# Kernel optimization log

Measured on AMD Instinct MI355X. Metric: run time of the kernel, lower is better.

## Reference

```python
import jax, jax.numpy as jnp
import numpy as np
from jax import lax

B, C_IN, T = 64, 16, 8192
HID, OUT = 64, 10
NEW_T = T // 4            # two MaxPool1d(2)
N_NODES = B * NEW_T       # 131072
N_EDGES = 2_097_152       # avg degree 16


def setup_inputs() -> dict:
    key = jax.random.key(0)
    ks = jax.random.split(key, 8)
    x = jax.random.normal(ks[0], (B, C_IN, T), dtype=jnp.float32)
    edge_index = jax.random.randint(ks[1], (2, N_EDGES), 0, N_NODES, dtype=jnp.int32)
    s = 0.05
    return {
        "x": x,
        "edge_index": edge_index,
        "conv1_w": jax.random.normal(ks[2], (16, C_IN, 5), dtype=jnp.float32) * s,
        "conv1_b": jnp.zeros((16,), jnp.float32),
        "conv2_w": jax.random.normal(ks[3], (32, 16, 5), dtype=jnp.float32) * s,
        "conv2_b": jnp.zeros((32,), jnp.float32),
        "gcn1_w": jax.random.normal(ks[4], (32, HID), dtype=jnp.float32) * s,
        "gcn1_b": jnp.zeros((HID,), jnp.float32),
        "gcn2_w": jax.random.normal(ks[5], (HID, HID), dtype=jnp.float32) * s,
        "gcn2_b": jnp.zeros((HID,), jnp.float32),
        "cls_w": jax.random.normal(ks[6], (HID, OUT), dtype=jnp.float32) * s,
        "cls_b": jnp.zeros((OUT,), jnp.float32),
    }


def conv1d(x, w, b):
    # x: [B, Cin, T], w: [Cout, Cin, K], padding=2 -> same length
    y = lax.conv_general_dilated(x, w, window_strides=(1,), padding=[(2, 2)],
                                 dimension_numbers=("NCH", "OIH", "NCH"))
    return y + b[None, :, None]


def maxpool2(x):
    # non-overlapping MaxPool1d(kernel=2) over last dim
    b, c, t = x.shape
    return x.reshape(b, c, t // 2, 2).max(axis=-1)


def gcn_conv(x, edge_index, W, b, n):
    # PyG GCNConv: add self-loops, symmetric normalization, scatter-add aggregate
    row, col = edge_index[0], edge_index[1]   # source j, target i
    loop = jnp.arange(n, dtype=row.dtype)
    row = jnp.concatenate([row, loop])
    col = jnp.concatenate([col, loop])
    deg = jax.ops.segment_sum(jnp.ones(row.shape, x.dtype), col, num_segments=n)
    dis = jnp.where(deg > 0, lax.rsqrt(deg), jnp.zeros_like(deg))
    norm = dis[row] * dis[col]                # [E+N]
    xw = x @ W                                # [N, out]
    msg = xw[row] * norm[:, None]             # gather along edges
    out = jax.ops.segment_sum(msg, col, num_segments=n)
    return out + b


def reference(x, edge_index, conv1_w, conv1_b, conv2_w, conv2_b,
              gcn1_w, gcn1_b, gcn2_w, gcn2_b, cls_w, cls_b):
    h = maxpool2(jax.nn.relu(conv1d(x, conv1_w, conv1_b)))     # [B,16,T/2]
    h = maxpool2(jax.nn.relu(conv1d(h, conv2_w, conv2_b)))     # [B,32,T/4]
    feat = h.transpose(0, 2, 1).reshape(-1, 32)                # [B*new_T, 32]
    n = feat.shape[0]
    g = jax.nn.relu(gcn_conv(feat, edge_index, gcn1_w, gcn1_b, n))
    g = jax.nn.relu(gcn_conv(g, edge_index, gcn2_w, gcn2_b, n))
    pooled = g.reshape(B, -1, HID).mean(axis=1)                # [B, HID]
    return pooled @ cls_w + cls_b                               # [B, OUT]
```

## Files before the change

### kernel.cpp

```cpp
#include <hip/hip_runtime.h>
#include <hip/hip_bf16.h>
#include <hip/hip_fp16.h>

#define BATCH 64
#define C_IN 16
#define T0 8192
#define T1 4096
#define T2 2048
#define N_NODES (BATCH * T2)
#define HID 64
#define NOUT 10

#define NCB 256
#define CB_SHIFT 9
#define CB_TGT 512
#define RCAP 9216
#define PC_EDGES 2048
#define PC_CAP 28

#define PK_RMASK 0x1FFFF

#define EC 1024

#define ZROW N_NODES

#define ROWW 24

#define FP8_SCALE 256.0f
#define FP8_SINV  (1.0f / 256.0f)

typedef __fp16 half8 __attribute__((ext_vector_type(8)));
typedef __fp16 half4v __attribute__((ext_vector_type(4)));
typedef float floatx4 __attribute__((ext_vector_type(4)));
typedef float floatx2 __attribute__((ext_vector_type(2)));

__global__ __launch_bounds__(256) void conv1_partition(
    const float* __restrict__ x, const float* __restrict__ w,
    const float* __restrict__ bias, __fp16* __restrict__ h1,
    const int* __restrict__ ei, int E,
    int* __restrict__ rcnt, int* __restrict__ gpairs,
    float* __restrict__ pool, unsigned char* __restrict__ xw,
    unsigned char* __restrict__ xw2) {
  __shared__ int smem_i[NCB + NCB * PC_CAP];
  if ((blockIdx.x & 1) == 0) {
    __fp16* xs = (__fp16*)smem_i;
    int bid = blockIdx.x >> 1;
    int b = bid >> 4;
    int tp0 = (bid & 15) * 256;
    if (bid == 0) {
      for (int k = threadIdx.x; k < BATCH * HID; k += 256) pool[k] = 0.f;
      if (threadIdx.x < 16) {
        ((unsigned*)(xw + (size_t)ZROW * 64))[threadIdx.x] = 0u;
        ((unsigned*)(xw2 + (size_t)ZROW * 64))[threadIdx.x] = 0u;
      }
    }
    int t_base = 2 * tp0 - 8;
    const float* xb = x + (size_t)b * C_IN * T0;
    {
      int ci = threadIdx.x >> 4;
      int l16 = threadIdx.x & 15;
      const float* xrow = xb + ci * T0;
      float4 va[4];
#pragma unroll
      for (int k = 0; k < 4; ++k) {
        int c4 = l16 + k * 16;
        int gt = t_base + c4 * 4;
        va[k] = make_float4(0.f, 0.f, 0.f, 0.f);
        if (gt >= 0 && gt + 4 <= T0) va[k] = *(const float4*)(xrow + gt);
      }
#pragma unroll
      for (int k = 0; k < 4; ++k) {
        int c4 = l16 + k * 16;
        __fp16* d = xs + (c4 * 4) * ROWW + ci;
        d[0] = (__fp16)va[k].x;
        d[ROWW] = (__fp16)va[k].y;
        d[2 * ROWW] = (__fp16)va[k].z;
        d[3 * ROWW] = (__fp16)va[k].w;
      }
      float4 vb[5];
      int okb[5];
#pragma unroll
      for (int k = 0; k < 5; ++k) {
        int c4 = l16 + (4 + k) * 16;
        okb[k] = (c4 < 132);
        int gt = t_base + c4 * 4;
        vb[k] = make_float4(0.f, 0.f, 0.f, 0.f);
        if (okb[k] && gt >= 0 && gt + 4 <= T0) vb[k] = *(const float4*)(xrow + gt);
      }
#pragma unroll
      for (int k = 0; k < 5; ++k) {
        if (okb[k]) {
          int c4 = l16 + (4 + k) * 16;
          __fp16* d = xs + (c4 * 4) * ROWW + ci;
          d[0] = (__fp16)vb[k].x;
          d[ROWW] = (__fp16)vb[k].y;
          d[2 * ROWW] = (__fp16)vb[k].z;
          d[3 * ROWW] = (__fp16)vb[k].w;
        }
      }
    }
    int ln = threadIdx.x & 15;
    int q = (threadIdx.x & 63) >> 4;
    int wib = threadIdx.x >> 6;
    half8 wb[3];
#pragma unroll
    for (int ks = 0; ks < 3; ++ks) {
      int kk = ks * 2 + (q >> 1);
#pragma unroll
      for (int j = 0; j < 8; ++j) {
        int ci = (q & 1) * 8 + j;
        float wv = (kk < 5) ? w[(ln * 16 + ci) * 5 + kk] : 0.f;
        wb[ks][j] = (__fp16)wv;
      }
    }
    float bv = bias[ln];
    __syncthreads();
    int qh = q >> 1, qo = (q & 1) * 8;
#pragma unroll 2
    for (int mtl = 0; mtl < 8; ++mtl) {
      int mt = wib * 8 + mtl;
      int posb = mt * 16 + ln + qh + 6;
      half8 a0 = *(const half8*)(xs + posb * ROWW + qo);
      half8 a1 = *(const half8*)(xs + (posb + 2) * ROWW + qo);
      half8 a2 = *(const half8*)(xs + (posb + 4) * ROWW + qo);
      floatx4 c0 = {0.f, 0.f, 0.f, 0.f};
      c0 = __builtin_amdgcn_mfma_f32_16x16x32_f16(a0, wb[0], c0, 0, 0, 0);
      c0 = __builtin_amdgcn_mfma_f32_16x16x32_f16(a1, wb[1], c0, 0, 0, 0);
      c0 = __builtin_amdgcn_mfma_f32_16x16x32_f16(a2, wb[2], c0, 0, 0, 0);
      int tp = tp0 + mt * 8 + q * 2;
      size_t o = ((size_t)b * T1 + tp) * 16 + ln;
      h1[o] = (__fp16)fmaxf(fmaxf(c0[0], c0[1]) + bv, 0.f);
      h1[o + 16] = (__fp16)fmaxf(fmaxf(c0[2], c0[3]) + bv, 0.f);
    }
  } else {
    int* lcnt = smem_i;
    int* lpk = smem_i + NCB;
    int pid = blockIdx.x >> 1;
    if (threadIdx.x < NCB) lcnt[threadIdx.x] = 0;
    __syncthreads();
    int e0 = pid * PC_EDGES;
    int rr[8], cc[8];
#pragma unroll
    for (int j = 0; j < 8; ++j) {
      int e = e0 + j * 256 + threadIdx.x;
      rr[j] = (e < E) ? ei[e] : 0;
      cc[j] = (e < E) ? ei[E + e] : -1;
    }
#pragma unroll
    for (int j = 0; j < 8; ++j) {
      if (cc[j] >= 0) {
        int cb = cc[j] >> CB_SHIFT;
        int pk = rr[j] | ((cc[j] & (CB_TGT - 1)) << 17);
        int slot = atomicAdd(&lcnt[cb], 1);
        if (slot < PC_CAP) {
          lpk[cb * PC_CAP + slot] = pk;
        } else {
          int pos = atomicAdd(&rcnt[cb], 1);
          if (pos < RCAP) gpairs[(size_t)cb * RCAP + pos] = pk;
        }
      }
    }
    __syncthreads();
    int t = threadIdx.x;
    if (t < NCB) {
      int n = lcnt[t];
      if (n > PC_CAP) n = PC_CAP;
      if (n > 0) {
        int base = atomicAdd(&rcnt[t], n);
        int* dst = gpairs + (size_t)t * RCAP;
        for (int k = 0; k < n; ++k) {
          int p = base + k;
          if (p < RCAP) dst[p] = lpk[t * PC_CAP + k];
        }
      }
    }
  }
}

__global__ __launch_bounds__(256) void conv2_gemm1(const __fp16* __restrict__ h1,
    const float* __restrict__ w, const float* __restrict__ bias,
    const float* __restrict__ W1, const float* __restrict__ dis,
    unsigned char* __restrict__ xw) {
  __shared__ __fp16 xs[520 * ROWW];
  __shared__ __fp16 fs[256 * 40];
  int b = blockIdx.x >> 3;
  int tp0 = (blockIdx.x & 7) * 256;
  int t_base = 2 * tp0 - 2;
  {
    half8 v[5];
    int row_[5], hf_[5], ok_[5];
#pragma unroll
    for (int k = 0; k < 5; ++k) {
      int idx = threadIdx.x + k * 256;
      ok_[k] = (idx < 520 * 2);
      int row = idx >> 1, hf = idx & 1;
      int gt = t_base + row;
      half8 z;
#pragma unroll
      for (int j = 0; j < 8; ++j) z[j] = (__fp16)0.f;
      v[k] = z;
      if (ok_[k] && gt >= 0 && gt < T1)
        v[k] = *(const half8*)(h1 + ((size_t)b * T1 + gt) * 16 + hf * 8);
      row_[k] = row; hf_[k] = hf;
    }
#pragma unroll
    for (int k = 0; k < 5; ++k)
      if (ok_[k]) *(half8*)(xs + row_[k] * ROWW + hf_[k] * 8) = v[k];
  }
  int ln = threadIdx.x & 15;
  int q = (threadIdx.x & 63) >> 4;
  int wib = threadIdx.x >> 6;
  half8 wb[2][3];
#pragma unroll
  for (int nt = 0; nt < 2; ++nt)
#pragma unroll
    for (int ks = 0; ks < 3; ++ks) {
      int kk = ks * 2 + (q >> 1);
#pragma unroll
      for (int j = 0; j < 8; ++j) {
        int ci = (q & 1) * 8 + j;
        float wv = (kk < 5) ? w[((nt * 16 + ln) * 16 + ci) * 5 + kk] : 0.f;
        wb[nt][ks][j] = (__fp16)wv;
      }
    }
  float b20 = bias[ln];
  float b21 = bias[16 + ln];
  __syncthreads();
  int qh = q >> 1, qo = (q & 1) * 8;
#pragma unroll 2
  for (int mtl = 0; mtl < 8; ++mtl) {
    int mt = wib * 8 + mtl;
    int posb = mt * 16 + ln + qh;
    half8 a0 = *(const half8*)(xs + posb * ROWW + qo);
    half8 a1 = *(const half8*)(xs + (posb + 2) * ROWW + qo);
    half8 a2 = *(const half8*)(xs + (posb + 4) * ROWW + qo);
    floatx4 c0 = {0.f, 0.f, 0.f, 0.f};
    floatx4 c1 = {0.f, 0.f, 0.f, 0.f};
    c0 = __builtin_amdgcn_mfma_f32_16x16x32_f16(a0, wb[0][0], c0, 0, 0, 0);
    c0 = __builtin_amdgcn_mfma_f32_16x16x32_f16(a1, wb[0][1], c0, 0, 0, 0);
    c0 = __builtin_amdgcn_mfma_f32_16x16x32_f16(a2, wb[0][2], c0, 0, 0, 0);
    c1 = __builtin_amdgcn_mfma_f32_16x16x32_f16(a0, wb[1][0], c1, 0, 0, 0);
    c1 = __builtin_amdgcn_mfma_f32_16x16x32_f16(a1, wb[1][1], c1, 0, 0, 0);
    c1 = __builtin_amdgcn_mfma_f32_16x16x32_f16(a2, wb[1][2], c1, 0, 0, 0);
    int node = wib * 64 + mtl * 8 + q * 2;
    fs[node * 40 + ln] = (__fp16)fmaxf(fmaxf(c0[0], c0[1]) + b20, 0.f);
    fs[(node + 1) * 40 + ln] = (__fp16)fmaxf(fmaxf(c0[2], c0[3]) + b20, 0.f);
    fs[node * 40 + 16 + ln] = (__fp16)fmaxf(fmaxf(c1[0], c1[1]) + b21, 0.f);
    fs[(node + 1) * 40 + 16 + ln] = (__fp16)fmaxf(fmaxf(c1[2], c1[3]) + b21, 0.f);
  }
  half8 bf[4];
#pragma unroll
  for (int t = 0; t < 4; ++t)
#pragma unroll
    for (int j = 0; j < 8; ++j)
      bf[t][j] = (__fp16)W1[(q * 8 + j) * 64 + ln * 4 + t];
  int gnode0 = b * T2 + tp0;
#pragma unroll
  for (int tt = 0; tt < 4; ++tt) {
    int lbase = (wib * 4 + tt) * 16;
    half8 a = *(const half8*)(fs + (lbase + ln) * 40 + q * 8);
    float d[4];
#pragma unroll
    for (int r = 0; r < 4; ++r) d[r] = dis[gnode0 + lbase + q * 4 + r] * FP8_SCALE;
    floatx4 acc[4];
#pragma unroll
    for (int t = 0; t < 4; ++t) {
      floatx4 z = {0.f, 0.f, 0.f, 0.f};
      acc[t] = __builtin_amdgcn_mfma_f32_16x16x32_f16(a, bf[t], z, 0, 0, 0);
    }
#pragma unroll
    for (int r = 0; r < 4; ++r) {
      int u = __builtin_amdgcn_cvt_pk_fp8_f32(acc[0][r] * d[r], acc[1][r] * d[r], 0, 0);
      u = __builtin_amdgcn_cvt_pk_fp8_f32(acc[2][r] * d[r], acc[3][r] * d[r], u, 1);
      *(unsigned*)(xw + (size_t)(gnode0 + lbase + q * 4 + r) * 64 + ln * 4) = (unsigned)u;
    }
  }
}

__global__ __launch_bounds__(512) void build_csr(const int* __restrict__ gpairs,
    const int* __restrict__ rcnt, int* __restrict__ ebuf,
    int* __restrict__ estart, int* __restrict__ ecnt, float* __restrict__ dis) {
  __shared__ int deg[CB_TGT];
  __shared__ int cur[CB_TGT];
  __shared__ int sc[CB_TGT];
  __shared__ int wsum[8];
  int b = blockIdx.x;
  int t = threadIdx.x;
  deg[t] = 0;
  cur[t] = 0;
  __syncthreads();
  int m = rcnt[b];
  if (m > RCAP) m = RCAP;
  const int* reg = gpairs + (size_t)b * RCAP;
  for (int k0 = 0; k0 < m; k0 += 2048) {
    int p[4], have[4];
#pragma unroll
    for (int u = 0; u < 4; ++u) {
      int k = k0 + u * 512 + t;
      have[u] = (k < m);
      p[u] = have[u] ? reg[k] : 0;
    }
#pragma unroll
    for (int u = 0; u < 4; ++u)
      if (have[u]) atomicAdd(&deg[(p[u] >> 17) & (CB_TGT - 1)], 1);
  }
  __syncthreads();
  int d = deg[t];
  int lane = t & 63;
  int wv = t >> 6;
  int sum = d;
#pragma unroll
  for (int off = 1; off < 64; off <<= 1) {
    int v = __shfl_up(sum, off, 64);
    if (lane >= off) sum += v;
  }
  if (lane == 63) wsum[wv] = sum;
  __syncthreads();
  int prefix = 0;
#pragma unroll
  for (int i = 0; i < 8; ++i) prefix += (i < wv) ? wsum[i] : 0;
  int excl = prefix + sum - d;
  int gi = (b << CB_SHIFT) + t;
  int base = b * RCAP;
  estart[gi] = base + excl;
  ecnt[gi] = d;
  dis[gi] = rsqrtf((float)d + 1.0f);
  sc[t] = excl;
  __syncthreads();
  for (int k0 = 0; k0 < m; k0 += 2048) {
    int p[4], have[4];
#pragma unroll
    for (int u = 0; u < 4; ++u) {
      int k = k0 + u * 512 + t;
      have[u] = (k < m);
      p[u] = have[u] ? reg[k] : 0;
    }
#pragma unroll
    for (int u = 0; u < 4; ++u) {
      if (have[u]) {
        int lc = (p[u] >> 17) & (CB_TGT - 1);
        int off = atomicAdd(&cur[lc], 1);
        ebuf[base + sc[lc] + off] = p[u] & PK_RMASK;
      }
    }
  }
}

#define LOADW(dst_, b0_)                                                        \
  _Pragma("unroll")                                                             \
  for (int j = 0; j < 4; ++j) {                                                 \
    unsigned r = (unsigned)sidx[(b0_) + j * 4];                                 \
    dst_[j] = *(const unsigned*)(tab + ((r << 6) + ch4));                       \
  }
#define LOADWT(dst_, stl_, s0_, c_)                                             \
  _Pragma("unroll")                                                             \
  for (int j = 0; j < 4; ++j) {                                                 \
    int k = (s0_) + j * 4 + es;                                                 \
    unsigned r = (unsigned)sidx[(stl_) + k];                                    \
    unsigned off = (k < (c_)) ? ((r << 6) + ch4) : zoff;                        \
    dst_[j] = *(const unsigned*)(tab + off);                                    \
  }
#define CONSW(src_, ALO, AHI)                                                   \
  _Pragma("unroll")                                                             \
  for (int j = 0; j < 4; ++j) {                                                 \
    ALO += __builtin_amdgcn_cvt_pk_f32_fp8(src_[j], 0);                         \
    AHI += __builtin_amdgcn_cvt_pk_f32_fp8(src_[j], 1);                         \
  }
#define GATHER_NODE(c_, stl_, ALO, AHI)                                         \
  {                                                                             \
    int sb_ = (stl_) + es;                                                      \
    int nt_ = ((c_) + 15) >> 4;                                                 \
    int nf_ = (c_) >> 4;                                                        \
    unsigned wa_[4], wb_[4];                                                    \
    if (nt_ > 0) {                                                              \
      if (nf_ > 0) { LOADW(wa_, sb_) } else { LOADWT(wa_, stl_, 0, c_) }        \
    }                                                                           \
    for (int w_ = 0; w_ < nt_; ++w_) {                                          \
      int n_ = w_ + 1;                                                          \
      if (n_ < nt_) {                                                           \
        if (w_ & 1) {                                                           \
          if (n_ < nf_) { LOADW(wa_, sb_ + (n_ << 4)) }                         \
          else { LOADWT(wa_, stl_, n_ << 4, c_) }                               \
        } else {                                                                \
          if (n_ < nf_) { LOADW(wb_, sb_ + (n_ << 4)) }                         \
          else { LOADWT(wb_, stl_, n_ << 4, c_) }                               \
        }                                                                       \
      }                                                                         \
      if (w_ & 1) { CONSW(wb_, ALO, AHI) } else { CONSW(wa_, ALO, AHI) }        \
    }                                                                           \
  }

#define STAGE_SIDX()                                                            \
  {                                                                             \
    int v0 = 0, v1 = 0, v2 = 0, v3 = 0;                                         \
    if (t < total) v0 = ebuf[span0 + t];                                        \
    if (t + 256 < total) v1 = ebuf[span0 + t + 256];                            \
    if (t + 512 < total) v2 = ebuf[span0 + t + 512];                            \
    if (t + 768 < total) v3 = ebuf[span0 + t + 768];                            \
    if (t < total) sidx[t] = v0;                                                \
    if (t + 256 < total) sidx[t + 256] = v1;                                    \
    if (t + 512 < total) sidx[t + 512] = v2;                                    \
    if (t + 768 < total) sidx[t + 768] = v3;                                    \
  }

__global__ __launch_bounds__(256) void agg1_gemm2(const unsigned char* __restrict__ tab,
    const int* __restrict__ ebuf, const int* __restrict__ estart,
    const int* __restrict__ ecnt, const float* __restrict__ dis,
    const float* __restrict__ bias, const float* __restrict__ W2,
    unsigned char* __restrict__ xw2, int N) {
  __shared__ __fp16 g1s[16 * 72];
  __shared__ int sidx[EC + 16];
  __shared__ int sst[16], scn[16];
  int t = threadIdx.x;
  int base16 = blockIdx.x * 16;
  if (t < 16) {
    sst[t] = estart[base16 + t];
    scn[t] = ecnt[base16 + t];
  }
  __syncthreads();
  int span0 = sst[0];
  int total = sst[15] + scn[15] - span0;
  if (total > EC) total = EC;
  STAGE_SIDX()
  __syncthreads();
  int lane = t & 63;
  int es = lane >> 4;
  int ch = lane & 15;
  int wib = t >> 6;
  unsigned ch4 = (unsigned)ch * 4u;
  unsigned zoff = ((unsigned)ZROW << 6) + ch4;
  float4 bv = *(const float4*)(bias + ch * 4);
  half8 b0, b1;
#pragma unroll
  for (int j = 0; j < 8; ++j) {
    b0[j] = (__fp16)W2[((lane >> 4) * 8 + j) * 64 + wib * 16 + (lane & 15)];
    b1[j] = (__fp16)W2[(32 + (lane >> 4) * 8 + j) * 64 + wib * 16 + (lane & 15)];
  }
  unsigned swv[4];
#pragma unroll
  for (int jj = 0; jj < 4; ++jj)
    swv[jj] = *(const unsigned*)(tab + (((unsigned)(base16 + wib * 4 + jj) << 6) + ch4));
#pragma unroll
  for (int jj = 0; jj < 4; ++jj) {
    int il = wib * 4 + jj;
    int i = base16 + il;
    int stl = sst[il] - span0;
    int c = scn[il];
    if (stl + c > EC) c = (EC > stl) ? (EC - stl) : 0;
    float di = dis[i] * FP8_SINV;
    floatx2 aLO = {0.f, 0.f}, aHI = {0.f, 0.f};
    GATHER_NODE(c, stl, aLO, aHI)
    float ax = aLO.x, ay = aLO.y, az = aHI.x, aw = aHI.y;
    ax += __shfl_xor(ax, 16, 64); ax += __shfl_xor(ax, 32, 64);
    ay += __shfl_xor(ay, 16, 64); ay += __shfl_xor(ay, 32, 64);
    az += __shfl_xor(az, 16, 64); az += __shfl_xor(az, 32, 64);
    aw += __shfl_xor(aw, 16, 64); aw += __shfl_xor(aw, 32, 64);
    floatx2 slo = __builtin_amdgcn_cvt_pk_f32_fp8(swv[jj], 0);
    floatx2 shi = __builtin_amdgcn_cvt_pk_f32_fp8(swv[jj], 1);
    if (es == 0) {
      half4v r;
      r[0] = (__fp16)fmaxf((ax + slo.x) * di + bv.x, 0.f);
      r[1] = (__fp16)fmaxf((ay + slo.y) * di + bv.y, 0.f);
      r[2] = (__fp16)fmaxf((az + shi.x) * di + bv.z, 0.f);
      r[3] = (__fp16)fmaxf((aw + shi.y) * di + bv.w, 0.f);
      *(half4v*)(g1s + il * 72 + ch * 4) = r;
    }
  }
  __syncthreads();
  int m = lane & 15;
  int q = lane >> 4;
  half8 a0 = *(const half8*)(g1s + m * 72 + q * 8);
  half8 a1 = *(const half8*)(g1s + m * 72 + 32 + q * 8);
  floatx4 acc = {0.f, 0.f, 0.f, 0.f};
  acc = __builtin_amdgcn_mfma_f32_16x16x32_f16(a0, b0, acc, 0, 0, 0);
  acc = __builtin_amdgcn_mfma_f32_16x16x32_f16(a1, b1, acc, 0, 0, 0);
  float sv[4];
#pragma unroll
  for (int r = 0; r < 4; ++r)
    sv[r] = acc[r] * dis[base16 + q * 4 + r] * FP8_SCALE;
  int u = __builtin_amdgcn_cvt_pk_fp8_f32(sv[0], sv[1], 0, 0);
  u = __builtin_amdgcn_cvt_pk_fp8_f32(sv[2], sv[3], u, 1);
#pragma unroll
  for (int r = 0; r < 4; ++r) {
    int node = base16 + q * 4 + r;
    xw2[(size_t)node * 64 + wib * 16 + m] = (unsigned char)(((unsigned)u) >> (8 * r));
  }
}

__global__ __launch_bounds__(256) void gcn_aggregate_pool(const unsigned char* __restrict__ tab,
    const int* __restrict__ ebuf, const int* __restrict__ estart,
    const int* __restrict__ ecnt, const float* __restrict__ dis,
    const float* __restrict__ bias, float* __restrict__ pool, int N) {
  __shared__ float4 red[4][16];
  __shared__ int sidx[EC + 16];
  __shared__ int sst[16], scn[16];
  int t = threadIdx.x;
  int base16 = blockIdx.x * 16;
  if (t < 16) {
    sst[t] = estart[base16 + t];
    scn[t] = ecnt[base16 + t];
  }
  __syncthreads();
  int span0 = sst[0];
  int total = sst[15] + scn[15] - span0;
  if (total > EC) total = EC;
  STAGE_SIDX()
  __syncthreads();
  int lane = t & 63;
  int es = lane >> 4;
  int ch = lane & 15;
  int wib = t >> 6;
  unsigned ch4 = (unsigned)ch * 4u;
  unsigned zoff = ((unsigned)ZROW << 6) + ch4;
  float4 bv = *(const float4*)(bias + ch * 4);
  unsigned swv[4];
#pragma unroll
  for (int jj = 0; jj < 4; ++jj)
    swv[jj] = *(const unsigned*)(tab + (((unsigned)(base16 + wib * 4 + jj) << 6) + ch4));
  float px = 0.f, py = 0.f, pz = 0.f, pw = 0.f;
#pragma unroll
  for (int jj = 0; jj < 4; ++jj) {
    int il = wib * 4 + jj;
    int i = base16 + il;
    int stl = sst[il] - span0;
    int c = scn[il];
    if (stl + c > EC) c = (EC > stl) ? (EC - stl) : 0;
    float di = dis[i] * FP8_SINV;
    floatx2 aLO = {0.f, 0.f}, aHI = {0.f, 0.f};
    GATHER_NODE(c, stl, aLO, aHI)
    float ax = aLO.x, ay = aLO.y, az = aHI.x, aw = aHI.y;
    ax += __shfl_xor(ax, 16, 64); ax += __shfl_xor(ax, 32, 64);
    ay += __shfl_xor(ay, 16, 64); ay += __shfl_xor(ay, 32, 64);
    az += __shfl_xor(az, 16, 64); az += __shfl_xor(az, 32, 64);
    aw += __shfl_xor(aw, 16, 64); aw += __shfl_xor(aw, 32, 64);
    floatx2 slo = __builtin_amdgcn_cvt_pk_f32_fp8(swv[jj], 0);
    floatx2 shi = __builtin_amdgcn_cvt_pk_f32_fp8(swv[jj], 1);
    px += fmaxf((ax + slo.x) * di + bv.x, 0.f);
    py += fmaxf((ay + slo.y) * di + bv.y, 0.f);
    pz += fmaxf((az + shi.x) * di + bv.z, 0.f);
    pw += fmaxf((aw + shi.y) * di + bv.w, 0.f);
  }
  if (es == 0) red[wib][ch] = make_float4(px, py, pz, pw);
  __syncthreads();
  if (threadIdx.x < 64) {
    int f = threadIdx.x;
    int c4 = f >> 2, j4 = f & 3;
    const float* r0 = (const float*)&red[0][c4];
    const float* r1 = (const float*)&red[1][c4];
    const float* r2 = (const float*)&red[2][c4];
    const float* r3 = (const float*)&red[3][c4];
    float sum = r0[j4] + r1[j4] + r2[j4] + r3[j4];
    int b = (blockIdx.x * 16) >> 11;
    atomicAdd(&pool[b * 64 + f], sum);
  }
}

__global__ __launch_bounds__(64) void classify(const float* __restrict__ pool,
    const float* __restrict__ cw, const float* __restrict__ cb,
    float* __restrict__ out) {
  __shared__ float pl[64];
  int b = blockIdx.x;
  int t = threadIdx.x;
  pl[t] = pool[b * 64 + t] * (1.0f / (float)T2);
  __syncthreads();
  if (t < NOUT) {
    float a = cb[t];
#pragma unroll
    for (int k = 0; k < 64; ++k) a += pl[k] * cw[k * NOUT + t];
    out[b * NOUT + t] = a;
  }
}

extern "C" void kernel_launch(void* const* d_in, const int* in_sizes, int n_in,
                              void* d_out, int out_size, void* d_ws, size_t ws_size,
                              hipStream_t stream) {
  const float* x    = (const float*)d_in[0];
  const int*   ei   = (const int*)d_in[1];
  const float* c1w  = (const float*)d_in[2];
  const float* c1b  = (const float*)d_in[3];
  const float* c2w  = (const float*)d_in[4];
  const float* c2b  = (const float*)d_in[5];
  const float* g1w  = (const float*)d_in[6];
  const float* g1b  = (const float*)d_in[7];
  const float* g2w  = (const float*)d_in[8];
  const float* g2b  = (const float*)d_in[9];
  const float* cw   = (const float*)d_in[10];
  const float* cb   = (const float*)d_in[11];
  float* out = (float*)d_out;
  int E = in_sizes[1] / 2;
  const int N = N_NODES;

  char* ws = (char*)d_ws;
  int*    gpairs = (int*)(ws);
  int*    ebuf   = (int*)(ws + 9437184);
  int*    rcnt   = (int*)(ws + 18874368);
  int*    estart = (int*)(ws + 18878464);
  int*    ecnt   = (int*)(ws + 19402752);
  float*  dis    = (float*)(ws + 19927040);
  float*  pool   = (float*)(ws + 20451328);
  unsigned char* xw  = (unsigned char*)(ws + 20467712);
  unsigned char* xw2 = (unsigned char*)(ws + 37245184);
  __fp16* h1     = (__fp16*)(ws + 54022656);

  hipMemsetAsync(rcnt, 0, NCB * sizeof(int), stream);

  conv1_partition<<<dim3(BATCH * 16 * 2), dim3(256), 0, stream>>>(
      x, c1w, c1b, h1, ei, E, rcnt, gpairs, pool, xw, xw2);

  build_csr<<<dim3(NCB), dim3(512), 0, stream>>>(gpairs, rcnt, ebuf, estart, ecnt, dis);

  conv2_gemm1<<<dim3(BATCH * 8), dim3(256), 0, stream>>>(h1, c2w, c2b, g1w, dis, xw);
  agg1_gemm2<<<dim3(N / 16), dim3(256), 0, stream>>>(xw, ebuf, estart, ecnt, dis, g1b, g2w, xw2, N);
  gcn_aggregate_pool<<<dim3(N / 16), dim3(256), 0, stream>>>(xw2, ebuf, estart, ecnt, dis, g2b, pool, N);

  classify<<<dim3(BATCH), dim3(64), 0, stream>>>(pool, cw, cb, out);
}
```

Before: 246.1 us.

## Fuse CSR build with conv2+GEMM1 via global degree atomics

```diff
diff --git a/kernel.cpp b/kernel.cpp
--- a/kernel.cpp
+++ b/kernel.cpp
@@ -39,6 +39,7 @@
     const float* __restrict__ bias, __fp16* __restrict__ h1,
     const int* __restrict__ ei, int E,
     int* __restrict__ rcnt, int* __restrict__ gpairs,
+    int* __restrict__ deg_g,
     float* __restrict__ pool, unsigned char* __restrict__ xw,
     unsigned char* __restrict__ xw2) {
   __shared__ int smem_i[NCB + NCB * PC_CAP];
@@ -127,7 +128,8 @@
       c0 = __builtin_amdgcn_mfma_f32_16x16x32_f16(a0, wb[0], c0, 0, 0, 0);
       c0 = __builtin_amdgcn_mfma_f32_16x16x32_f16(a1, wb[1], c0, 0, 0, 0);
       c0 = __builtin_amdgcn_mfma_f32_16x16x32_f16(a2, wb[2], c0, 0, 0, 0);
-      int tp = tp0 + mt * 8 + q * 2;
+      int tp = tp0 + mtl * 8 + q * 2 + wib * 64;
+      tp = tp0 + mt * 8 + q * 2;
       size_t o = ((size_t)b * T1 + tp) * 16 + ln;
       h1[o] = (__fp16)fmaxf(fmaxf(c0[0], c0[1]) + bv, 0.f);
       h1[o + 16] = (__fp16)fmaxf(fmaxf(c0[2], c0[3]) + bv, 0.f);
@@ -149,6 +151,7 @@
 #pragma unroll
     for (int j = 0; j < 8; ++j) {
       if (cc[j] >= 0) {
+        atomicAdd(&deg_g[cc[j]], 1);
         int cb = cc[j] >> CB_SHIFT;
         int pk = rr[j] | ((cc[j] & (CB_TGT - 1)) << 17);
         int slot = atomicAdd(&lcnt[cb], 1);
@@ -177,170 +180,176 @@
   }
 }
 
-__global__ __launch_bounds__(256) void conv2_gemm1(const __fp16* __restrict__ h1,
-    const float* __restrict__ w, const float* __restrict__ bias,
-    const float* __restrict__ W1, const float* __restrict__ dis,
-    unsigned char* __restrict__ xw) {
-  __shared__ __fp16 xs[520 * ROWW];
-  __shared__ __fp16 fs[256 * 40];
-  int b = blockIdx.x >> 3;
-  int tp0 = (blockIdx.x & 7) * 256;
-  int t_base = 2 * tp0 - 2;
-  {
-    half8 v[5];
-    int row_[5], hf_[5], ok_[5];
-#pragma unroll
-    for (int k = 0; k < 5; ++k) {
-      int idx = threadIdx.x + k * 256;
-      ok_[k] = (idx < 520 * 2);
-      int row = idx >> 1, hf = idx & 1;
-      int gt = t_base + row;
-      half8 z;
-#pragma unroll
-      for (int j = 0; j < 8; ++j) z[j] = (__fp16)0.f;
-      v[k] = z;
-      if (ok_[k] && gt >= 0 && gt < T1)
-        v[k] = *(const half8*)(h1 + ((size_t)b * T1 + gt) * 16 + hf * 8);
-      row_[k] = row; hf_[k] = hf;
-    }
-#pragma unroll
-    for (int k = 0; k < 5; ++k)
-      if (ok_[k]) *(half8*)(xs + row_[k] * ROWW + hf_[k] * 8) = v[k];
-  }
-  int ln = threadIdx.x & 15;
-  int q = (threadIdx.x & 63) >> 4;
-  int wib = threadIdx.x >> 6;
-  half8 wb[2][3];
-#pragma unroll
-  for (int nt = 0; nt < 2; ++nt)
-#pragma unroll
-    for (int ks = 0; ks < 3; ++ks) {
-      int kk = ks * 2 + (q >> 1);
-#pragma unroll
-      for (int j = 0; j < 8; ++j) {
-        int ci = (q & 1) * 8 + j;
-        float wv = (kk < 5) ? w[((nt * 16 + ln) * 16 + ci) * 5 + kk] : 0.f;
-        wb[nt][ks][j] = (__fp16)wv;
-      }
-    }
-  float b20 = bias[ln];
-  float b21 = bias[16 + ln];
-  __syncthreads();
-  int qh = q >> 1, qo = (q & 1) * 8;
-#pragma unroll 2
-  for (int mtl = 0; mtl < 8; ++mtl) {
-    int mt = wib * 8 + mtl;
-    int posb = mt * 16 + ln + qh;
-    half8 a0 = *(const half8*)(xs + posb * ROWW + qo);
-    half8 a1 = *(const half8*)(xs + (posb + 2) * ROWW + qo);
-    half8 a2 = *(const half8*)(xs + (posb + 4) * ROWW + qo);
-    floatx4 c0 = {0.f, 0.f, 0.f, 0.f};
-    floatx4 c1 = {0.f, 0.f, 0.f, 0.f};
-    c0 = __builtin_amdgcn_mfma_f32_16x16x32_f16(a0, wb[0][0], c0, 0, 0, 0);
-    c0 = __builtin_amdgcn_mfma_f32_16x16x32_f16(a1, wb[0][1], c0, 0, 0, 0);
-    c0 = __builtin_amdgcn_mfma_f32_16x16x32_f16(a2, wb[0][2], c0, 0, 0, 0);
-    c1 = __builtin_amdgcn_mfma_f32_16x16x32_f16(a0, wb[1][0], c1, 0, 0, 0);
-    c1 = __builtin_amdgcn_mfma_f32_16x16x32_f16(a1, wb[1][1], c1, 0, 0, 0);
-    c1 = __builtin_amdgcn_mfma_f32_16x16x32_f16(a2, wb[1][2], c1, 0, 0, 0);
-    int node = wib * 64 + mtl * 8 + q * 2;
-    fs[node * 40 + ln] = (__fp16)fmaxf(fmaxf(c0[0], c0[1]) + b20, 0.f);
-    fs[(node + 1) * 40 + ln] = (__fp16)fmaxf(fmaxf(c0[2], c0[3]) + b20, 0.f);
-    fs[node * 40 + 16 + ln] = (__fp16)fmaxf(fmaxf(c1[0], c1[1]) + b21, 0.f);
-    fs[(node + 1) * 40 + 16 + ln] = (__fp16)fmaxf(fmaxf(c1[2], c1[3]) + b21, 0.f);
-  }
-  half8 bf[4];
-#pragma unroll
-  for (int t = 0; t < 4; ++t)
-#pragma unroll
-    for (int j = 0; j < 8; ++j)
-      bf[t][j] = (__fp16)W1[(q * 8 + j) * 64 + ln * 4 + t];
-  int gnode0 = b * T2 + tp0;
-#pragma unroll
-  for (int tt = 0; tt < 4; ++tt) {
-    int lbase = (wib * 4 + tt) * 16;
-    half8 a = *(const half8*)(fs + (lbase + ln) * 40 + q * 8);
-    float d[4];
-#pragma unroll
-    for (int r = 0; r < 4; ++r) d[r] = dis[gnode0 + lbase + q * 4 + r] * FP8_SCALE;
-    floatx4 acc[4];
-#pragma unroll
-    for (int t = 0; t < 4; ++t) {
-      floatx4 z = {0.f, 0.f, 0.f, 0.f};
-      acc[t] = __builtin_amdgcn_mfma_f32_16x16x32_f16(a, bf[t], z, 0, 0, 0);
-    }
-#pragma unroll
-    for (int r = 0; r < 4; ++r) {
-      int u = __builtin_amdgcn_cvt_pk_fp8_f32(acc[0][r] * d[r], acc[1][r] * d[r], 0, 0);
-      u = __builtin_amdgcn_cvt_pk_fp8_f32(acc[2][r] * d[r], acc[3][r] * d[r], u, 1);
-      *(unsigned*)(xw + (size_t)(gnode0 + lbase + q * 4 + r) * 64 + ln * 4) = (unsigned)u;
-    }
-  }
-}
-
-__global__ __launch_bounds__(512) void build_csr(const int* __restrict__ gpairs,
+__global__ __launch_bounds__(512) void csr_conv2(const int* __restrict__ gpairs,
     const int* __restrict__ rcnt, int* __restrict__ ebuf,
-    int* __restrict__ estart, int* __restrict__ ecnt, float* __restrict__ dis) {
-  __shared__ int deg[CB_TGT];
-  __shared__ int cur[CB_TGT];
-  __shared__ int sc[CB_TGT];
-  __shared__ int wsum[8];
-  int b = blockIdx.x;
-  int t = threadIdx.x;
-  deg[t] = 0;
-  cur[t] = 0;
-  __syncthreads();
-  int m = rcnt[b];
-  if (m > RCAP) m = RCAP;
-  const int* reg = gpairs + (size_t)b * RCAP;
-  for (int k0 = 0; k0 < m; k0 += 2048) {
-    int p[4], have[4];
-#pragma unroll
-    for (int u = 0; u < 4; ++u) {
-      int k = k0 + u * 512 + t;
-      have[u] = (k < m);
-      p[u] = have[u] ? reg[k] : 0;
-    }
-#pragma unroll
-    for (int u = 0; u < 4; ++u)
-      if (have[u]) atomicAdd(&deg[(p[u] >> 17) & (CB_TGT - 1)], 1);
-  }
-  __syncthreads();
-  int d = deg[t];
-  int lane = t & 63;
-  int wv = t >> 6;
-  int sum = d;
-#pragma unroll
-  for (int off = 1; off < 64; off <<= 1) {
-    int v = __shfl_up(sum, off, 64);
-    if (lane >= off) sum += v;
-  }
-  if (lane == 63) wsum[wv] = sum;
-  __syncthreads();
-  int prefix = 0;
-#pragma unroll
-  for (int i = 0; i < 8; ++i) prefix += (i < wv) ? wsum[i] : 0;
-  int excl = prefix + sum - d;
-  int gi = (b << CB_SHIFT) + t;
-  int base = b * RCAP;
-  estart[gi] = base + excl;
-  ecnt[gi] = d;
-  dis[gi] = rsqrtf((float)d + 1.0f);
-  sc[t] = excl;
-  __syncthreads();
-  for (int k0 = 0; k0 < m; k0 += 2048) {
-    int p[4], have[4];
-#pragma unroll
-    for (int u = 0; u < 4; ++u) {
-      int k = k0 + u * 512 + t;
-      have[u] = (k < m);
-      p[u] = have[u] ? reg[k] : 0;
-    }
-#pragma unroll
-    for (int u = 0; u < 4; ++u) {
-      if (have[u]) {
-        int lc = (p[u] >> 17) & (CB_TGT - 1);
-        int off = atomicAdd(&cur[lc], 1);
-        ebuf[base + sc[lc] + off] = p[u] & PK_RMASK;
+    int* __restrict__ estart, int* __restrict__ ecnt, float* __restrict__ dis,
+    const __fp16* __restrict__ h1, const float* __restrict__ w,
+    const float* __restrict__ bias, const float* __restrict__ W1,
+    const int* __restrict__ deg_g, unsigned char* __restrict__ xw) {
+  __shared__ int smem_i[11616];
+  int bid = blockIdx.x;
+  if (bid % 3 == 0) {
+    int* deg = smem_i;
+    int* cur = smem_i + 512;
+    int* sc = smem_i + 1024;
+    int* wsum = smem_i + 1536;
+    int b = bid / 3;
+    int t = threadIdx.x;
+    deg[t] = 0;
+    cur[t] = 0;
+    __syncthreads();
+    int m = rcnt[b];
+    if (m > RCAP) m = RCAP;
+    const int* reg = gpairs + (size_t)b * RCAP;
+    for (int k0 = 0; k0 < m; k0 += 2048) {
+      int p[4], have[4];
+#pragma unroll
+      for (int u = 0; u < 4; ++u) {
+        int k = k0 + u * 512 + t;
+        have[u] = (k < m);
+        p[u] = have[u] ? reg[k] : 0;
+      }
+#pragma unroll
+      for (int u = 0; u < 4; ++u)
+        if (have[u]) atomicAdd(&deg[(p[u] >> 17) & (CB_TGT - 1)], 1);
+    }
+    __syncthreads();
+    int d = deg[t];
+    int lane = t & 63;
+    int wv = t >> 6;
+    int sum = d;
+#pragma unroll
+    for (int off = 1; off < 64; off <<= 1) {
+      int v = __shfl_up(sum, off, 64);
+      if (lane >= off) sum += v;
+    }
+    if (lane == 63) wsum[wv] = sum;
+    __syncthreads();
+    int prefix = 0;
+#pragma unroll
+    for (int i = 0; i < 8; ++i) prefix += (i < wv) ? wsum[i] : 0;
+    int excl = prefix + sum - d;
+    int gi = (b << CB_SHIFT) + t;
+    int base = b * RCAP;
+    estart[gi] = base + excl;
+    ecnt[gi] = d;
+    dis[gi] = rsqrtf((float)d + 1.0f);
+    sc[t] = excl;
+    __syncthreads();
+    for (int k0 = 0; k0 < m; k0 += 2048) {
+      int p[4], have[4];
+#pragma unroll
+      for (int u = 0; u < 4; ++u) {
+        int k = k0 + u * 512 + t;
+        have[u] = (k < m);
+        p[u] = have[u] ? reg[k] : 0;
+      }
+#pragma unroll
+      for (int u = 0; u < 4; ++u) {
+        if (have[u]) {
+          int lc = (p[u] >> 17) & (CB_TGT - 1);
+          int off = atomicAdd(&cur[lc], 1);
+          ebuf[base + sc[lc] + off] = p[u] & PK_RMASK;
+        }
+      }
+    }
+  } else {
+    __fp16* xs = (__fp16*)smem_i;
+    __fp16* fs = (__fp16*)(smem_i + 6240);
+    float* disl = (float*)(smem_i + 11360);
+    int cid = bid - bid / 3 - 1;
+    int b = cid >> 3;
+    int tp0 = (cid & 7) * 256;
+    int t = threadIdx.x;
+    int t_base = 2 * tp0 - 2;
+    int gnode0 = b * T2 + tp0;
+    if (t < 256) disl[t] = rsqrtf((float)deg_g[gnode0 + t] + 1.0f) * FP8_SCALE;
+    {
+      half8 v[3];
+      int row_[3], hf_[3], ok_[3];
+#pragma unroll
+      for (int k = 0; k < 3; ++k) {
+        int idx = t + k * 512;
+        ok_[k] = (idx < 520 * 2);
+        int row = idx >> 1, hf = idx & 1;
+        int gt = t_base + row;
+        half8 z;
+#pragma unroll
+        for (int j = 0; j < 8; ++j) z[j] = (__fp16)0.f;
+        v[k] = z;
+        if (ok_[k] && gt >= 0 && gt < T1)
+          v[k] = *(const half8*)(h1 + ((size_t)b * T1 + gt) * 16 + hf * 8);
+        row_[k] = row; hf_[k] = hf;
+      }
+#pragma unroll
+      for (int k = 0; k < 3; ++k)
+        if (ok_[k]) *(half8*)(xs + row_[k] * ROWW + hf_[k] * 8) = v[k];
+    }
+    int ln = t & 15;
+    int q = (t & 63) >> 4;
+    int wib = t >> 6;
+    half8 wb[2][3];
+#pragma unroll
+    for (int nt = 0; nt < 2; ++nt)
+#pragma unroll
+      for (int ks = 0; ks < 3; ++ks) {
+        int kk = ks * 2 + (q >> 1);
+#pragma unroll
+        for (int j = 0; j < 8; ++j) {
+          int ci = (q & 1) * 8 + j;
+          float wv = (kk < 5) ? w[((nt * 16 + ln) * 16 + ci) * 5 + kk] : 0.f;
+          wb[nt][ks][j] = (__fp16)wv;
+        }
+      }
+    float b20 = bias[ln];
+    float b21 = bias[16 + ln];
+    __syncthreads();
+    int qh = q >> 1, qo = (q & 1) * 8;
+#pragma unroll
+    for (int mtl = 0; mtl < 4; ++mtl) {
+      int mt = wib * 4 + mtl;
+      int posb = mt * 16 + ln + qh;
+      half8 a0 = *(const half8*)(xs + posb * ROWW + qo);
+      half8 a1 = *(const half8*)(xs + (posb + 2) * ROWW + qo);
+      half8 a2 = *(const half8*)(xs + (posb + 4) * ROWW + qo);
+      floatx4 c0 = {0.f, 0.f, 0.f, 0.f};
+      floatx4 c1 = {0.f, 0.f, 0.f, 0.f};
+      c0 = __builtin_amdgcn_mfma_f32_16x16x32_f16(a0, wb[0][0], c0, 0, 0, 0);
+      c0 = __builtin_amdgcn_mfma_f32_16x16x32_f16(a1, wb[0][1], c0, 0, 0, 0);
+      c0 = __builtin_amdgcn_mfma_f32_16x16x32_f16(a2, wb[0][2], c0, 0, 0, 0);
+      c1 = __builtin_amdgcn_mfma_f32_16x16x32_f16(a0, wb[1][0], c1, 0, 0, 0);
+      c1 = __builtin_amdgcn_mfma_f32_16x16x32_f16(a1, wb[1][1], c1, 0, 0, 0);
+      c1 = __builtin_amdgcn_mfma_f32_16x16x32_f16(a2, wb[1][2], c1, 0, 0, 0);
+      int node = mt * 8 + q * 2;
+      fs[node * 40 + ln] = (__fp16)fmaxf(fmaxf(c0[0], c0[1]) + b20, 0.f);
+      fs[(node + 1) * 40 + ln] = (__fp16)fmaxf(fmaxf(c0[2], c0[3]) + b20, 0.f);
+      fs[node * 40 + 16 + ln] = (__fp16)fmaxf(fmaxf(c1[0], c1[1]) + b21, 0.f);
+      fs[(node + 1) * 40 + 16 + ln] = (__fp16)fmaxf(fmaxf(c1[2], c1[3]) + b21, 0.f);
+    }
+    half8 bf[4];
+#pragma unroll
+    for (int tc = 0; tc < 4; ++tc)
+#pragma unroll
+      for (int j = 0; j < 8; ++j)
+        bf[tc][j] = (__fp16)W1[(q * 8 + j) * 64 + ln * 4 + tc];
+#pragma unroll
+    for (int tt = 0; tt < 2; ++tt) {
+      int lbase = (wib * 2 + tt) * 16;
+      half8 a = *(const half8*)(fs + (lbase + ln) * 40 + q * 8);
+      float d[4];
+#pragma unroll
+      for (int r = 0; r < 4; ++r) d[r] = disl[lbase + q * 4 + r];
+      floatx4 acc[4];
+#pragma unroll
+      for (int tc = 0; tc < 4; ++tc) {
+        floatx4 z = {0.f, 0.f, 0.f, 0.f};
+        acc[tc] = __builtin_amdgcn_mfma_f32_16x16x32_f16(a, bf[tc], z, 0, 0, 0);
+      }
+#pragma unroll
+      for (int r = 0; r < 4; ++r) {
+        int u = __builtin_amdgcn_cvt_pk_fp8_f32(acc[0][r] * d[r], acc[1][r] * d[r], 0, 0);
+        u = __builtin_amdgcn_cvt_pk_fp8_f32(acc[2][r] * d[r], acc[3][r] * d[r], u, 1);
+        *(unsigned*)(xw + (size_t)(gnode0 + lbase + q * 4 + r) * 64 + ln * 4) = (unsigned)u;
       }
     }
   }
@@ -599,17 +608,19 @@
   float*  dis    = (float*)(ws + 19927040);
   float*  pool   = (float*)(ws + 20451328);
   unsigned char* xw  = (unsigned char*)(ws + 20467712);
+  int*    deg_g  = (int*)(ws + 28856384);
   unsigned char* xw2 = (unsigned char*)(ws + 37245184);
   __fp16* h1     = (__fp16*)(ws + 54022656);
 
   hipMemsetAsync(rcnt, 0, NCB * sizeof(int), stream);
+  hipMemsetAsync(deg_g, 0, N_NODES * sizeof(int), stream);
 
   conv1_partition<<<dim3(BATCH * 16 * 2), dim3(256), 0, stream>>>(
-      x, c1w, c1b, h1, ei, E, rcnt, gpairs, pool, xw, xw2);
-
-  build_csr<<<dim3(NCB), dim3(512), 0, stream>>>(gpairs, rcnt, ebuf, estart, ecnt, dis);
-
-  conv2_gemm1<<<dim3(BATCH * 8), dim3(256), 0, stream>>>(h1, c2w, c2b, g1w, dis, xw);
+      x, c1w, c1b, h1, ei, E, rcnt, gpairs, deg_g, pool, xw, xw2);
+
+  csr_conv2<<<dim3(NCB * 3), dim3(512), 0, stream>>>(
+      gpairs, rcnt, ebuf, estart, ecnt, dis, h1, c2w, c2b, g1w, deg_g, xw);
+
   agg1_gemm2<<<dim3(N / 16), dim3(256), 0, stream>>>(xw, ebuf, estart, ecnt, dis, g1b, g2w, xw2, N);
   gcn_aggregate_pool<<<dim3(N / 16), dim3(256), 0, stream>>>(xw2, ebuf, estart, ecnt, dis, g2b, pool, N);
 
```

New measurement: 323.3 us. 31.4% more time.
